# Kernel optimization log

Hardware: AMD Instinct MI355X
Metric: run time of the kernel (lower is better)

The kernel has to match this reference:

```python
import jax, jax.numpy as jnp
import numpy as np

B, S, D, H = 2, 2048, 1024, 16
HD = D // H  # head dim = 64


def setup_inputs() -> dict:
    key = jax.random.key(0)
    k0, k1, k2 = jax.random.split(key, 3)
    x = jax.random.normal(k0, (B, S, D), dtype=jnp.float32)
    # fused QKV projection: nn.Linear(D, 3D) -> weight [3D, D], bias [3D]
    Wqkv_w = jax.random.normal(k1, (3 * D, D), dtype=jnp.float32) * (1.0 / np.sqrt(D))
    Wqkv_b = jnp.zeros((3 * D,), dtype=jnp.float32)
    out_w = jax.random.normal(k2, (D, D), dtype=jnp.float32) * (1.0 / np.sqrt(D))
    out_b = jnp.zeros((D,), dtype=jnp.float32)
    # ALiBi-like additive bias, shape [1, H, 1, S] (broadcasts over queries)
    slopes = 2.0 ** (-8.0 * jnp.arange(1, H + 1, dtype=jnp.float32) / H)  # [H]
    dist = (S - 1) - jnp.arange(S, dtype=jnp.float32)                      # [S]
    attn_bias = (-slopes[:, None] * dist[None, :]).reshape(1, H, 1, S)
    # key padding mask: second sequence is padded by 256 tokens at the end
    lengths = jnp.array([S, S - 256])
    attention_mask = jnp.arange(S)[None, :] < lengths[:, None]             # [B, S] bool
    return {"x": x, "Wqkv_w": Wqkv_w, "Wqkv_b": Wqkv_b, "out_w": out_w,
            "out_b": out_b, "attn_bias": attn_bias, "attention_mask": attention_mask}


def reference(x, Wqkv_w, Wqkv_b, out_w, out_b, attn_bias, attention_mask):
    b, s, d = x.shape
    # fused QKV projection, then chunk into q, k, v along feature dim
    qkv = jnp.einsum('bsd,ed->bse', x, Wqkv_w) + Wqkv_b  # [b, s, 3d]
    q, k, v = jnp.split(qkv, 3, axis=-1)
    # b s (h hd) -> b h s hd
    q = q.reshape(b, s, H, HD).transpose(0, 2, 1, 3)
    k = k.reshape(b, s, H, HD).transpose(0, 2, 1, 3)
    v = v.reshape(b, s, H, HD).transpose(0, 2, 1, 3)
    softmax_scale = 1.0 / np.sqrt(HD)
    aw = jnp.einsum('bhqe,bhke->bhqk', q, k) * softmax_scale  # [b, H, s, s]
    aw = aw + attn_bias  # attn_bias broadcasts [1,H,1,s] -> [b,H,s,s]
    min_val = jnp.finfo(aw.dtype).min
    # key padding mask: mask positions where attention_mask is False
    aw = jnp.where(attention_mask[:, None, None, :], aw, min_val)
    # causal mask (is_causal=True, s_q == s_k)
    causal = jnp.tril(jnp.ones((s, s), dtype=bool))
    aw = jnp.where(causal[None, None, :, :], aw, min_val)
    p = jax.nn.softmax(aw, axis=-1)
    out = jnp.einsum('bhqk,bhke->bhqe', p, v)  # [b, H, s, HD]
    out = out.transpose(0, 2, 1, 3).reshape(b, s, d)
    return jnp.einsum('bsd,ed->bse', out, out_w) + out_b
```

## Files before the change

kernel.cpp:

```cpp
#include <hip/hip_runtime.h>
#include <hip/hip_bf16.h>
#include <stdint.h>

typedef __attribute__((ext_vector_type(8))) short s16x8;
typedef __attribute__((ext_vector_type(8))) unsigned short u16x8;
typedef __attribute__((ext_vector_type(4))) float f32x4;

#define SEQ 2048
#define LOG2E 1.44269504088896f

__device__ __forceinline__ unsigned short f2b(float x) {
  union { __hip_bfloat16 h; unsigned short u; } cv;
  cv.h = __float2bfloat16(x);
  return cv.u;
}

__device__ __forceinline__ float exp2fast(float x) {
  float r;
  asm("v_exp_f32 %0, %1" : "=v"(r) : "v"(x));
  return r;
}

__device__ __forceinline__ void gload16(const void* g, void* l) {
  __builtin_amdgcn_global_load_lds(
      (const __attribute__((address_space(1))) void*)g,
      (__attribute__((address_space(3))) void*)l, 16, 0, 0);
}

__global__ void cvt_all(const float* __restrict__ x, const float* __restrict__ wq,
                        const float* __restrict__ ow, __hip_bfloat16* __restrict__ xb,
                        __hip_bfloat16* __restrict__ wqb, __hip_bfloat16* __restrict__ owb) {
  const int i = blockIdx.x * 256 + threadIdx.x;
  const float* src;
  __hip_bfloat16* dst;
  int off;
  if (i < 1048576) { src = x; dst = xb; off = i; }
  else if (i < 1835008) { src = wq; dst = wqb; off = i - 1048576; }
  else { src = ow; dst = owb; off = i - 1835008; }
  float4 v = reinterpret_cast<const float4*>(src)[off];
  ushort4 o;
  o.x = f2b(v.x); o.y = f2b(v.y); o.z = f2b(v.z); o.w = f2b(v.w);
  reinterpret_cast<ushort4*>(dst)[off] = o;
}

__global__ void build_biasm(const float* __restrict__ abias,
                            const void* __restrict__ maskp,
                            float* __restrict__ biasm) {
  const int i = blockIdx.x * 256 + threadIdx.x;
  const int b = i >> 15, h = (i >> 11) & 15, kv = i & 2047;
  const int* mi = (const int*)maskp;
  const unsigned char* mb = (const unsigned char*)maskp;
  const bool int_fmt = (mi[0] == 0 || mi[0] == 1);
  const bool ok = int_fmt ? (mi[b * SEQ + kv] != 0) : (mb[b * SEQ + kv] != 0);
  biasm[i] = ok ? abias[h * SEQ + kv] * LOG2E : -1e30f;
}

template <int MODE, int BM>
__global__ __launch_bounds__(256) void gemm_bt(
    const __hip_bfloat16* __restrict__ A, const __hip_bfloat16* __restrict__ B,
    const float* __restrict__ bias, void* __restrict__ Cout,
    __hip_bfloat16* __restrict__ Vt, int M, int N, int K) {
  constexpr int MR = BM / 32;
  __shared__ __align__(16) __hip_bfloat16 As[BM * 32];
  __shared__ __align__(16) __hip_bfloat16 Bs[128 * 32];
  const int tid = threadIdx.x;
  const int lane = tid & 63;
  const int w = tid >> 6;
  const int wr = w >> 1, wc = w & 1;
  const int rowg = blockIdx.x * BM;
  const int colg = blockIdx.y * 128;
  const int lr = lane & 15;
  const int lk = (lane >> 4) * 8;
  f32x4 acc[MR][4];
#pragma unroll
  for (int m = 0; m < MR; ++m)
#pragma unroll
    for (int n = 0; n < 4; ++n) acc[m][n] = (f32x4){0.f, 0.f, 0.f, 0.f};
  for (int kt = 0; kt < K; kt += 32) {
#pragma unroll
    for (int r = 0; r < BM / 64; ++r) {
      const int idx = r * 256 + tid;
      gload16(A + (size_t)(rowg + (idx >> 2)) * K + kt + (idx & 3) * 8, As + idx * 8);
    }
#pragma unroll
    for (int r = 0; r < 2; ++r) {
      const int idx = r * 256 + tid;
      gload16(B + (size_t)(colg + (idx >> 2)) * K + kt + (idx & 3) * 8, Bs + idx * 8);
    }
    __syncthreads();
    s16x8 af[MR], bfr[4];
#pragma unroll
    for (int m = 0; m < MR; ++m)
      af[m] = *reinterpret_cast<const s16x8*>(As + (wr * (BM / 2) + m * 16 + lr) * 32 + lk);
#pragma unroll
    for (int n = 0; n < 4; ++n)
      bfr[n] = *reinterpret_cast<const s16x8*>(Bs + (wc * 64 + n * 16 + lr) * 32 + lk);
#pragma unroll
    for (int m = 0; m < MR; ++m)
#pragma unroll
      for (int n = 0; n < 4; ++n)
        acc[m][n] = __builtin_amdgcn_mfma_f32_16x16x32_bf16(af[m], bfr[n], acc[m][n], 0, 0, 0);
    __syncthreads();
  }
  const int r0l = (lane >> 4) * 4;
#pragma unroll
  for (int m = 0; m < MR; ++m) {
#pragma unroll
    for (int n = 0; n < 4; ++n) {
      const int col = colg + wc * 64 + n * 16 + lr;
      const int row0 = rowg + wr * (BM / 2) + m * 16 + r0l;
      const float bv = bias[col];
      if (MODE == 0) {
        if (col < 2048) {
          __hip_bfloat16* qkb = (__hip_bfloat16*)Cout;
#pragma unroll
          for (int j = 0; j < 4; ++j)
            qkb[(size_t)(row0 + j) * 2048 + col] = __float2bfloat16(acc[m][n][j] + bv);
        } else {
          const int c2 = col - 2048;
          const int bb = row0 >> 11;
          const int s0 = row0 & 2047;
          ushort4 pk;
          unsigned short* pp = (unsigned short*)&pk;
#pragma unroll
          for (int j = 0; j < 4; ++j) pp[j] = f2b(acc[m][n][j] + bv);
          *reinterpret_cast<ushort4*>(
              Vt + ((size_t)(bb * 16 + (c2 >> 6)) * 64 + (c2 & 63)) * 2048 + s0) = pk;
        }
      } else {
        float* o = (float*)Cout;
#pragma unroll
        for (int j = 0; j < 4; ++j)
          o[(size_t)(row0 + j) * N + col] = acc[m][n][j] + bv;
      }
    }
  }
}

__device__ __forceinline__ int swz(int row, int byteInRow) {
  return row * 128 + (byteInRow ^ ((row & 7) << 4));
}

__device__ __forceinline__ void attn_tile(
    const char* Ks, const char* Vs, char* pw, const float* Bm,
    s16x8 aq0, s16x8 aq1, int lane, int kv0, int q_abs, bool causal,
    float& m_r, float& l_r, f32x4* oa) {
  const int lr = lane & 15;
  const int g = lane >> 4;
  const int lkB = g * 16;
  const float SCALE2 = 0.125f * LOG2E;
  f32x4 sf[4];
#pragma unroll
  for (int n = 0; n < 4; ++n) {
    s16x8 ak0 = *reinterpret_cast<const s16x8*>(Ks + swz(n * 16 + lr, lkB));
    s16x8 ak1 = *reinterpret_cast<const s16x8*>(Ks + swz(n * 16 + lr, 64 + lkB));
    f32x4 z = (f32x4){0.f, 0.f, 0.f, 0.f};
    z = __builtin_amdgcn_mfma_f32_16x16x32_bf16(ak0, aq0, z, 0, 0, 0);
    z = __builtin_amdgcn_mfma_f32_16x16x32_bf16(ak1, aq1, z, 0, 0, 0);
    sf[n] = z;
  }
#pragma unroll
  for (int n = 0; n < 4; ++n) {
    f32x4 bv = *reinterpret_cast<const f32x4*>(Bm + n * 16 + g * 4);
#pragma unroll
    for (int j = 0; j < 4; ++j) sf[n][j] = fmaf(sf[n][j], SCALE2, bv[j]);
  }
  if (causal) {
    const int kvb = kv0 + g * 4;
#pragma unroll
    for (int n = 0; n < 4; ++n)
#pragma unroll
      for (int j = 0; j < 4; ++j)
        if (kvb + n * 16 + j > q_abs) sf[n][j] = -1e30f;
  }
  float mx[4];
#pragma unroll
  for (int n = 0; n < 4; ++n)
    mx[n] = fmaxf(fmaxf(sf[n][0], sf[n][1]), fmaxf(sf[n][2], sf[n][3]));
  float tm = fmaxf(fmaxf(mx[0], mx[1]), fmaxf(mx[2], mx[3]));
  tm = fmaxf(tm, __shfl_xor(tm, 16));
  tm = fmaxf(tm, __shfl_xor(tm, 32));
  const float mn = fmaxf(m_r, tm);
  const float al = exp2fast(m_r - mn);
  m_r = mn;
  float ps[4];
#pragma unroll
  for (int n = 0; n < 4; ++n) {
#pragma unroll
    for (int j = 0; j < 4; ++j) sf[n][j] = exp2fast(sf[n][j] - mn);
    ps[n] = (sf[n][0] + sf[n][1]) + (sf[n][2] + sf[n][3]);
  }
  float rs = (ps[0] + ps[1]) + (ps[2] + ps[3]);
  rs += __shfl_xor(rs, 16);
  rs += __shfl_xor(rs, 32);
  l_r = l_r * al + rs;
  float alj[4];
#pragma unroll
  for (int j = 0; j < 4; ++j) alj[j] = __shfl(al, g * 4 + j);
#pragma unroll
  for (int d = 0; d < 4; ++d)
#pragma unroll
    for (int j = 0; j < 4; ++j) oa[d][j] *= alj[j];
#pragma unroll
  for (int n = 0; n < 4; ++n) {
    union { ushort4 u; uint2 v; } pk;
    pk.u.x = f2b(sf[n][0]); pk.u.y = f2b(sf[n][1]);
    pk.u.z = f2b(sf[n][2]); pk.u.w = f2b(sf[n][3]);
    *reinterpret_cast<uint2*>(pw + lr * 128 + ((n * 32 + g * 8) ^ ((lr & 7) << 4))) = pk.v;
  }
  s16x8 pa0 = *reinterpret_cast<const s16x8*>(pw + swz(lr, lkB));
  s16x8 pa1 = *reinterpret_cast<const s16x8*>(pw + swz(lr, 64 + lkB));
#pragma unroll
  for (int d = 0; d < 4; ++d) {
    s16x8 bv0 = *reinterpret_cast<const s16x8*>(Vs + swz(d * 16 + lr, lkB));
    s16x8 bv1 = *reinterpret_cast<const s16x8*>(Vs + swz(d * 16 + lr, 64 + lkB));
    oa[d] = __builtin_amdgcn_mfma_f32_16x16x32_bf16(pa0, bv0, oa[d], 0, 0, 0);
    oa[d] = __builtin_amdgcn_mfma_f32_16x16x32_bf16(pa1, bv1, oa[d], 0, 0, 0);
  }
}

__global__ __launch_bounds__(512) void attn_fwd3(
    const __hip_bfloat16* __restrict__ qk, const __hip_bfloat16* __restrict__ Vt,
    const float* __restrict__ biasm, __hip_bfloat16* __restrict__ O) {
  __shared__ __align__(16) char KV[2][2][64 * 128];
  __shared__ __align__(16) char Ps[8][16 * 128];
  __shared__ float Bm[2][64];
  __shared__ float mlArr[4][2][16];
  const int tid = threadIdx.x;
  const int lane = tid & 63;
  const int w = tid >> 6;
  const int wsub = w & 3;
  const int z = w >> 2;
  const int bid = blockIdx.x;
  const int qt = 31 - (bid >> 5);
  const int bh = bid & 31;
  const int b = bh >> 4, h = bh & 15;
  const int row0 = qt * 64 + wsub * 16;
  const int lr = lane & 15;
  const int g = lane >> 4;
  const int NTit = (qt >> 1) + 1;
  const __hip_bfloat16* qbase = qk + (size_t)b * SEQ * 2048 + h * 64 + g * 8;
  const s16x8 aq0 = *reinterpret_cast<const s16x8*>(qbase + (size_t)(row0 + lr) * 2048);
  const s16x8 aq1 = *reinterpret_cast<const s16x8*>(qbase + (size_t)(row0 + lr) * 2048 + 32);
  const int q_abs = row0 + lr;
  float m_r = -INFINITY, l_r = 0.f;
  f32x4 oa[4];
#pragma unroll
  for (int d = 0; d < 4; ++d) oa[d] = (f32x4){0.f, 0.f, 0.f, 0.f};
  const int srow = tid >> 3;
  const int c8 = tid & 7;
  const __hip_bfloat16* kbase = qk + (size_t)b * SEQ * 2048 + 1024 + h * 64 + c8 * 8;
  const __hip_bfloat16* vbase = Vt + ((size_t)bh * 64 + srow) * 2048 + c8 * 8;
  const float* bmb = biasm + (size_t)bh * 2048;
  u16x8 kpe, kpo, vpe, vpo;
  float bmv = 0.f;
#define ISSUE(T)                                                                 \
  {                                                                              \
    const int tE_ = 2 * (T);                                                     \
    const int tO_ = (2 * (T) + 1 <= qt) ? (2 * (T) + 1) : qt;                    \
    kpe = *reinterpret_cast<const u16x8*>(kbase + (size_t)(tE_ * 64 + srow) * 2048); \
    kpo = *reinterpret_cast<const u16x8*>(kbase + (size_t)(tO_ * 64 + srow) * 2048); \
    vpe = *reinterpret_cast<const u16x8*>(vbase + tE_ * 64);                     \
    vpo = *reinterpret_cast<const u16x8*>(vbase + tO_ * 64);                     \
    if (tid < 64) bmv = bmb[tE_ * 64 + tid];                                     \
    else if (tid < 128) bmv = bmb[tO_ * 64 + (tid - 64)];                        \
  }
  ISSUE(0);
  for (int t = 0; t < NTit; ++t) {
    __syncthreads();
    *reinterpret_cast<u16x8*>(KV[0][0] + swz(srow, c8 * 16)) = kpe;
    *reinterpret_cast<u16x8*>(KV[1][0] + swz(srow, c8 * 16)) = kpo;
    *reinterpret_cast<u16x8*>(KV[0][1] + swz(srow, c8 * 16)) = vpe;
    *reinterpret_cast<u16x8*>(KV[1][1] + swz(srow, c8 * 16)) = vpo;
    if (tid < 64) Bm[0][tid] = bmv;
    else if (tid < 128) Bm[1][tid - 64] = bmv;
    __syncthreads();
    if (t + 1 < NTit) ISSUE(t + 1);
    const int tz = 2 * t + z;
    if (tz <= qt)
      attn_tile(KV[z][0], KV[z][1], Ps[w], Bm[z], aq0, aq1, lane,
                tz * 64, q_abs, tz == qt, m_r, l_r, oa);
  }
#undef ISSUE
  __syncthreads();
  if (z == 1) {
    float* mo = (float*)(&Ps[0][0] + wsub * 4096);
#pragma unroll
    for (int d = 0; d < 4; ++d)
#pragma unroll
      for (int j = 0; j < 4; ++j)
        mo[(g * 4 + j) * 64 + d * 16 + lr] = oa[d][j];
    if (lane < 16) {
      mlArr[wsub][0][lr] = m_r;
      mlArr[wsub][1][lr] = l_r;
    }
  }
  __syncthreads();
  if (z == 0) {
    const float mB = mlArr[wsub][0][lr];
    const float lB = mlArr[wsub][1][lr];
    const float mS = fmaxf(m_r, mB);
    const float fA = exp2fast(m_r - mS);
    const float fB = exp2fast(mB - mS);
    const float linv = 1.0f / (l_r * fA + lB * fB);
    float fAj[4], fBj[4], lij[4];
#pragma unroll
    for (int j = 0; j < 4; ++j) {
      fAj[j] = __shfl(fA, g * 4 + j);
      fBj[j] = __shfl(fB, g * 4 + j);
      lij[j] = __shfl(linv, g * 4 + j);
    }
    const float* mo = (const float*)(&Ps[0][0] + wsub * 4096);
#pragma unroll
    for (int d = 0; d < 4; ++d)
#pragma unroll
      for (int j = 0; j < 4; ++j) {
        const float v =
            (oa[d][j] * fAj[j] + mo[(g * 4 + j) * 64 + d * 16 + lr] * fBj[j]) * lij[j];
        O[(size_t)(b * SEQ + row0 + g * 4 + j) * 1024 + h * 64 + d * 16 + lr] =
            __float2bfloat16(v);
      }
  }
}

extern "C" void kernel_launch(void* const* d_in, const int* in_sizes, int n_in,
                              void* d_out, int out_size, void* d_ws, size_t ws_size,
                              hipStream_t stream) {
  const float* x     = (const float*)d_in[0];
  const float* wqkv  = (const float*)d_in[1];
  const float* bqkv  = (const float*)d_in[2];
  const float* wout  = (const float*)d_in[3];
  const float* bout  = (const float*)d_in[4];
  const float* abias = (const float*)d_in[5];
  const void*  mask  = d_in[6];

  __hip_bfloat16* ws  = (__hip_bfloat16*)d_ws;
  __hip_bfloat16* xb  = ws;
  __hip_bfloat16* wqb = ws + 4194304;
  __hip_bfloat16* owb = ws + 7340032;
  __hip_bfloat16* qkb = ws + 8388608;
  __hip_bfloat16* vtb = ws + 16777216;
  float*          bmf = (float*)(ws + 20971520);
  __hip_bfloat16* aob = xb;

  cvt_all<<<8192, 256, 0, stream>>>(x, wqkv, wout, xb, wqb, owb);
  build_biasm<<<256, 256, 0, stream>>>(abias, mask, bmf);
  gemm_bt<0, 128><<<dim3(32, 24), 256, 0, stream>>>(xb, wqb, bqkv, (void*)qkb, vtb,
                                                    4096, 3072, 1024);
  attn_fwd3<<<1024, 512, 0, stream>>>(qkb, vtb, bmf, aob);
  gemm_bt<1, 64><<<dim3(64, 8), 256, 0, stream>>>(aob, owb, bout, d_out,
                                                  (__hip_bfloat16*)nullptr, 4096, 1024, 1024);
}
```

Baseline: 122.1 us.

## Pair causal query tiles per block for balanced attention work; fuse bias-mask build

Each attention block now processes two query tiles (qt=31-p and qt=p), so every block does the same 17 KV-pair iterations instead of a varying count. The grid drops from 1024 blocks to 512, and the K/V prefetch pipeline carries straight across the tile switch, with a merge-and-write step in between. The separate build_biasm kernel is folded into cvt_all as extra blocks, removing one kernel launch. The trade-off is fewer, longer blocks, which removes tail imbalance but may lower occupancy-driven latency hiding.

New measurement: 125.4 us. 1.03x slower.

```diff
diff --git a/kernel.cpp b/kernel.cpp
--- a/kernel.cpp
+++ b/kernel.cpp
@@ -28,9 +28,21 @@
 }
 
 __global__ void cvt_all(const float* __restrict__ x, const float* __restrict__ wq,
-                        const float* __restrict__ ow, __hip_bfloat16* __restrict__ xb,
-                        __hip_bfloat16* __restrict__ wqb, __hip_bfloat16* __restrict__ owb) {
+                        const float* __restrict__ ow, const float* __restrict__ abias,
+                        const void* __restrict__ maskp,
+                        __hip_bfloat16* __restrict__ xb, __hip_bfloat16* __restrict__ wqb,
+                        __hip_bfloat16* __restrict__ owb, float* __restrict__ biasm) {
   const int i = blockIdx.x * 256 + threadIdx.x;
+  if (i >= 2097152) {
+    const int j = i - 2097152;
+    const int b = j >> 15, h = (j >> 11) & 15, kv = j & 2047;
+    const int* mi = (const int*)maskp;
+    const unsigned char* mb = (const unsigned char*)maskp;
+    const bool int_fmt = (mi[0] == 0 || mi[0] == 1);
+    const bool ok = int_fmt ? (mi[b * SEQ + kv] != 0) : (mb[b * SEQ + kv] != 0);
+    biasm[j] = ok ? abias[h * SEQ + kv] * LOG2E : -1e30f;
+    return;
+  }
   const float* src;
   __hip_bfloat16* dst;
   int off;
@@ -41,18 +53,6 @@
   ushort4 o;
   o.x = f2b(v.x); o.y = f2b(v.y); o.z = f2b(v.z); o.w = f2b(v.w);
   reinterpret_cast<ushort4*>(dst)[off] = o;
-}
-
-__global__ void build_biasm(const float* __restrict__ abias,
-                            const void* __restrict__ maskp,
-                            float* __restrict__ biasm) {
-  const int i = blockIdx.x * 256 + threadIdx.x;
-  const int b = i >> 15, h = (i >> 11) & 15, kv = i & 2047;
-  const int* mi = (const int*)maskp;
-  const unsigned char* mb = (const unsigned char*)maskp;
-  const bool int_fmt = (mi[0] == 0 || mi[0] == 1);
-  const bool ok = int_fmt ? (mi[b * SEQ + kv] != 0) : (mb[b * SEQ + kv] != 0);
-  biasm[i] = ok ? abias[h * SEQ + kv] * LOG2E : -1e30f;
 }
 
 template <int MODE, int BM>
@@ -219,7 +219,7 @@
   }
 }
 
-__global__ __launch_bounds__(512) void attn_fwd3(
+__global__ __launch_bounds__(512) void attn_fwd4(
     const __hip_bfloat16* __restrict__ qk, const __hip_bfloat16* __restrict__ Vt,
     const float* __restrict__ biasm, __hip_bfloat16* __restrict__ O) {
   __shared__ __align__(16) char KV[2][2][64 * 128];
@@ -231,18 +231,19 @@
   const int w = tid >> 6;
   const int wsub = w & 3;
   const int z = w >> 2;
-  const int bid = blockIdx.x;
-  const int qt = 31 - (bid >> 5);
-  const int bh = bid & 31;
+  const int p = blockIdx.x;
+  const int bh = blockIdx.y;
   const int b = bh >> 4, h = bh & 15;
-  const int row0 = qt * 64 + wsub * 16;
   const int lr = lane & 15;
   const int g = lane >> 4;
-  const int NTit = (qt >> 1) + 1;
+  const int qtA = 31 - p, qtB = p;
+  const int NT_A = (qtA >> 1) + 1;
   const __hip_bfloat16* qbase = qk + (size_t)b * SEQ * 2048 + h * 64 + g * 8;
-  const s16x8 aq0 = *reinterpret_cast<const s16x8*>(qbase + (size_t)(row0 + lr) * 2048);
-  const s16x8 aq1 = *reinterpret_cast<const s16x8*>(qbase + (size_t)(row0 + lr) * 2048 + 32);
-  const int q_abs = row0 + lr;
+  int qcur = qtA;
+  int row0 = qtA * 64 + wsub * 16;
+  int q_abs = row0 + lr;
+  s16x8 aq0 = *reinterpret_cast<const s16x8*>(qbase + (size_t)(row0 + lr) * 2048);
+  s16x8 aq1 = *reinterpret_cast<const s16x8*>(qbase + (size_t)(row0 + lr) * 2048 + 32);
   float m_r = -INFINITY, l_r = 0.f;
   f32x4 oa[4];
 #pragma unroll
@@ -254,10 +255,10 @@
   const float* bmb = biasm + (size_t)bh * 2048;
   u16x8 kpe, kpo, vpe, vpo;
   float bmv = 0.f;
-#define ISSUE(T)                                                                 \
+#define ISSUE(TL, QQ)                                                            \
   {                                                                              \
-    const int tE_ = 2 * (T);                                                     \
-    const int tO_ = (2 * (T) + 1 <= qt) ? (2 * (T) + 1) : qt;                    \
+    const int tE_ = 2 * (TL);                                                    \
+    const int tO_ = (2 * (TL) + 1 <= (QQ)) ? (2 * (TL) + 1) : (QQ);              \
     kpe = *reinterpret_cast<const u16x8*>(kbase + (size_t)(tE_ * 64 + srow) * 2048); \
     kpo = *reinterpret_cast<const u16x8*>(kbase + (size_t)(tO_ * 64 + srow) * 2048); \
     vpe = *reinterpret_cast<const u16x8*>(vbase + tE_ * 64);                     \
@@ -265,8 +266,44 @@
     if (tid < 64) bmv = bmb[tE_ * 64 + tid];                                     \
     else if (tid < 128) bmv = bmb[tO_ * 64 + (tid - 64)];                        \
   }
-  ISSUE(0);
-  for (int t = 0; t < NTit; ++t) {
+#define MERGE_WRITE()                                                            \
+  {                                                                              \
+    __syncthreads();                                                             \
+    if (z == 1) {                                                                \
+      float* mo = (float*)(&Ps[0][0] + wsub * 4096);                             \
+      _Pragma("unroll") for (int d = 0; d < 4; ++d)                              \
+          _Pragma("unroll") for (int j = 0; j < 4; ++j)                          \
+              mo[(g * 4 + j) * 64 + d * 16 + lr] = oa[d][j];                     \
+      if (lane < 16) { mlArr[wsub][0][lr] = m_r; mlArr[wsub][1][lr] = l_r; }     \
+    }                                                                            \
+    __syncthreads();                                                             \
+    if (z == 0) {                                                                \
+      const float mB = mlArr[wsub][0][lr];                                       \
+      const float lB = mlArr[wsub][1][lr];                                       \
+      const float mS = fmaxf(m_r, mB);                                           \
+      const float fA = exp2fast(m_r - mS);                                       \
+      const float fB = exp2fast(mB - mS);                                        \
+      const float linv = 1.0f / (l_r * fA + lB * fB);                            \
+      float fAj[4], fBj[4], lij[4];                                              \
+      _Pragma("unroll") for (int j = 0; j < 4; ++j) {                            \
+        fAj[j] = __shfl(fA, g * 4 + j);                                          \
+        fBj[j] = __shfl(fB, g * 4 + j);                                          \
+        lij[j] = __shfl(linv, g * 4 + j);                                        \
+      }                                                                          \
+      const float* mo = (const float*)(&Ps[0][0] + wsub * 4096);                 \
+      _Pragma("unroll") for (int d = 0; d < 4; ++d)                              \
+          _Pragma("unroll") for (int j = 0; j < 4; ++j) {                        \
+            const float v = (oa[d][j] * fAj[j] +                                 \
+                             mo[(g * 4 + j) * 64 + d * 16 + lr] * fBj[j]) * lij[j]; \
+            O[(size_t)(b * SEQ + row0 + g * 4 + j) * 1024 + h * 64 + d * 16 + lr] = \
+                __float2bfloat16(v);                                             \
+          }                                                                      \
+    }                                                                            \
+  }
+  ISSUE(0, qtA);
+  for (int t = 0; t < 17; ++t) {
+    const bool inA = t < NT_A;
+    const int tl = inA ? t : t - NT_A;
     __syncthreads();
     *reinterpret_cast<u16x8*>(KV[0][0] + swz(srow, c8 * 16)) = kpe;
     *reinterpret_cast<u16x8*>(KV[1][0] + swz(srow, c8 * 16)) = kpo;
@@ -275,52 +312,31 @@
     if (tid < 64) Bm[0][tid] = bmv;
     else if (tid < 128) Bm[1][tid - 64] = bmv;
     __syncthreads();
-    if (t + 1 < NTit) ISSUE(t + 1);
-    const int tz = 2 * t + z;
-    if (tz <= qt)
+    if (t + 1 < 17) {
+      const bool inA2 = (t + 1) < NT_A;
+      const int tl2 = inA2 ? t + 1 : t + 1 - NT_A;
+      const int q2 = inA2 ? qtA : qtB;
+      ISSUE(tl2, q2);
+    }
+    const int tz = 2 * tl + z;
+    if (tz <= qcur)
       attn_tile(KV[z][0], KV[z][1], Ps[w], Bm[z], aq0, aq1, lane,
-                tz * 64, q_abs, tz == qt, m_r, l_r, oa);
-  }
+                tz * 64, q_abs, tz == qcur, m_r, l_r, oa);
+    if (t == NT_A - 1) {
+      MERGE_WRITE();
+      qcur = qtB;
+      row0 = qtB * 64 + wsub * 16;
+      q_abs = row0 + lr;
+      aq0 = *reinterpret_cast<const s16x8*>(qbase + (size_t)(row0 + lr) * 2048);
+      aq1 = *reinterpret_cast<const s16x8*>(qbase + (size_t)(row0 + lr) * 2048 + 32);
+      m_r = -INFINITY; l_r = 0.f;
+#pragma unroll
+      for (int d = 0; d < 4; ++d) oa[d] = (f32x4){0.f, 0.f, 0.f, 0.f};
+    }
+  }
+  MERGE_WRITE();
 #undef ISSUE
-  __syncthreads();
-  if (z == 1) {
-    float* mo = (float*)(&Ps[0][0] + wsub * 4096);
-#pragma unroll
-    for (int d = 0; d < 4; ++d)
-#pragma unroll
-      for (int j = 0; j < 4; ++j)
-        mo[(g * 4 + j) * 64 + d * 16 + lr] = oa[d][j];
-    if (lane < 16) {
-      mlArr[wsub][0][lr] = m_r;
-      mlArr[wsub][1][lr] = l_r;
-    }
-  }
-  __syncthreads();
-  if (z == 0) {
-    const float mB = mlArr[wsub][0][lr];
-    const float lB = mlArr[wsub][1][lr];
-    const float mS = fmaxf(m_r, mB);
-    const float fA = exp2fast(m_r - mS);
-    const float fB = exp2fast(mB - mS);
-    const float linv = 1.0f / (l_r * fA + lB * fB);
-    float fAj[4], fBj[4], lij[4];
-#pragma unroll
-    for (int j = 0; j < 4; ++j) {
-      fAj[j] = __shfl(fA, g * 4 + j);
-      fBj[j] = __shfl(fB, g * 4 + j);
-      lij[j] = __shfl(linv, g * 4 + j);
-    }
-    const float* mo = (const float*)(&Ps[0][0] + wsub * 4096);
-#pragma unroll
-    for (int d = 0; d < 4; ++d)
-#pragma unroll
-      for (int j = 0; j < 4; ++j) {
-        const float v =
-            (oa[d][j] * fAj[j] + mo[(g * 4 + j) * 64 + d * 16 + lr] * fBj[j]) * lij[j];
-        O[(size_t)(b * SEQ + row0 + g * 4 + j) * 1024 + h * 64 + d * 16 + lr] =
-            __float2bfloat16(v);
-      }
-  }
+#undef MERGE_WRITE
 }
 
 extern "C" void kernel_launch(void* const* d_in, const int* in_sizes, int n_in,
@@ -343,11 +359,10 @@
   float*          bmf = (float*)(ws + 20971520);
   __hip_bfloat16* aob = xb;
 
-  cvt_all<<<8192, 256, 0, stream>>>(x, wqkv, wout, xb, wqb, owb);
-  build_biasm<<<256, 256, 0, stream>>>(abias, mask, bmf);
+  cvt_all<<<8448, 256, 0, stream>>>(x, wqkv, wout, abias, mask, xb, wqb, owb, bmf);
   gemm_bt<0, 128><<<dim3(32, 24), 256, 0, stream>>>(xb, wqb, bqkv, (void*)qkb, vtb,
                                                     4096, 3072, 1024);
-  attn_fwd3<<<1024, 512, 0, stream>>>(qkb, vtb, bmf, aob);
+  attn_fwd4<<<dim3(16, 32), 512, 0, stream>>>(qkb, vtb, bmf, aob);
   gemm_bt<1, 64><<<dim3(64, 8), 256, 0, stream>>>(aob, owb, bout, d_out,
                                                   (__hip_bfloat16*)nullptr, 4096, 1024, 1024);
 }
```

## Restructure attention: 128-row query tiles, direct-to-LDS K/V loads, fused bias prep

Applied to the files above, without the earlier changes.

The attention kernel now gives each 512-thread block 128 query rows (16 per wave) instead of splitting 64 rows across two KV-parity wave groups. This removes the end-of-kernel merge of two partial softmax states. K and V tiles are double-buffered with global_load_lds direct-to-LDS copies, which needs the QKV GEMM epilogue to write K and V pre-swizzled in global memory. The bias/mask build is merged into the conversion kernel to save a launch, and the bias is now read from global memory rather than staged in LDS. The costs are more per-wave idle time on the causal diagonal and a more complex block-to-tile mapping with reversed ordering for load balance.

After: 133.7 us. 9.5% more time.

```diff
diff --git a/kernel.cpp b/kernel.cpp
--- a/kernel.cpp
+++ b/kernel.cpp
@@ -28,9 +28,21 @@
 }
 
 __global__ void cvt_all(const float* __restrict__ x, const float* __restrict__ wq,
-                        const float* __restrict__ ow, __hip_bfloat16* __restrict__ xb,
-                        __hip_bfloat16* __restrict__ wqb, __hip_bfloat16* __restrict__ owb) {
+                        const float* __restrict__ ow, const float* __restrict__ abias,
+                        const void* __restrict__ maskp,
+                        __hip_bfloat16* __restrict__ xb, __hip_bfloat16* __restrict__ wqb,
+                        __hip_bfloat16* __restrict__ owb, float* __restrict__ biasm) {
   const int i = blockIdx.x * 256 + threadIdx.x;
+  if (i >= 2097152) {
+    const int j = i - 2097152;
+    const int b = j >> 15, h = (j >> 11) & 15, kv = j & 2047;
+    const int* mi = (const int*)maskp;
+    const unsigned char* mb = (const unsigned char*)maskp;
+    const bool int_fmt = (mi[0] == 0 || mi[0] == 1);
+    const bool ok = int_fmt ? (mi[b * SEQ + kv] != 0) : (mb[b * SEQ + kv] != 0);
+    biasm[j] = ok ? abias[h * SEQ + kv] * LOG2E : -1e30f;
+    return;
+  }
   const float* src;
   __hip_bfloat16* dst;
   int off;
@@ -41,18 +53,6 @@
   ushort4 o;
   o.x = f2b(v.x); o.y = f2b(v.y); o.z = f2b(v.z); o.w = f2b(v.w);
   reinterpret_cast<ushort4*>(dst)[off] = o;
-}
-
-__global__ void build_biasm(const float* __restrict__ abias,
-                            const void* __restrict__ maskp,
-                            float* __restrict__ biasm) {
-  const int i = blockIdx.x * 256 + threadIdx.x;
-  const int b = i >> 15, h = (i >> 11) & 15, kv = i & 2047;
-  const int* mi = (const int*)maskp;
-  const unsigned char* mb = (const unsigned char*)maskp;
-  const bool int_fmt = (mi[0] == 0 || mi[0] == 1);
-  const bool ok = int_fmt ? (mi[b * SEQ + kv] != 0) : (mb[b * SEQ + kv] != 0);
-  biasm[i] = ok ? abias[h * SEQ + kv] * LOG2E : -1e30f;
 }
 
 template <int MODE, int BM>
@@ -111,21 +111,31 @@
       const int row0 = rowg + wr * (BM / 2) + m * 16 + r0l;
       const float bv = bias[col];
       if (MODE == 0) {
-        if (col < 2048) {
-          __hip_bfloat16* qkb = (__hip_bfloat16*)Cout;
+        __hip_bfloat16* qkb = (__hip_bfloat16*)Cout;
+        if (col < 1024) {
 #pragma unroll
           for (int j = 0; j < 4; ++j)
             qkb[(size_t)(row0 + j) * 2048 + col] = __float2bfloat16(acc[m][n][j] + bv);
+        } else if (col < 2048) {
+          const int dd = col & 63;
+          const int base = col - dd;
+#pragma unroll
+          for (int j = 0; j < 4; ++j) {
+            const int s = row0 + j;
+            qkb[(size_t)s * 2048 + base + (dd ^ ((s & 7) << 3))] =
+                __float2bfloat16(acc[m][n][j] + bv);
+          }
         } else {
           const int c2 = col - 2048;
+          const int dd = c2 & 63;
           const int bb = row0 >> 11;
-          const int s0 = row0 & 2047;
+          const int s0 = (row0 & 2047) ^ ((dd & 7) << 3);
           ushort4 pk;
           unsigned short* pp = (unsigned short*)&pk;
 #pragma unroll
           for (int j = 0; j < 4; ++j) pp[j] = f2b(acc[m][n][j] + bv);
           *reinterpret_cast<ushort4*>(
-              Vt + ((size_t)(bb * 16 + (c2 >> 6)) * 64 + (c2 & 63)) * 2048 + s0) = pk;
+              Vt + ((size_t)(bb * 16 + (c2 >> 6)) * 64 + dd) * 2048 + s0) = pk;
         }
       } else {
         float* o = (float*)Cout;
@@ -142,7 +152,7 @@
 }
 
 __device__ __forceinline__ void attn_tile(
-    const char* Ks, const char* Vs, char* pw, const float* Bm,
+    const char* Ks, const char* Vs, char* pw, const float* bmb,
     s16x8 aq0, s16x8 aq1, int lane, int kv0, int q_abs, bool causal,
     float& m_r, float& l_r, f32x4* oa) {
   const int lr = lane & 15;
@@ -161,7 +171,7 @@
   }
 #pragma unroll
   for (int n = 0; n < 4; ++n) {
-    f32x4 bv = *reinterpret_cast<const f32x4*>(Bm + n * 16 + g * 4);
+    f32x4 bv = *reinterpret_cast<const f32x4*>(bmb + kv0 + n * 16 + g * 4);
 #pragma unroll
     for (int j = 0; j < 4; ++j) sf[n][j] = fmaf(sf[n][j], SCALE2, bv[j]);
   }
@@ -219,108 +229,67 @@
   }
 }
 
-__global__ __launch_bounds__(512) void attn_fwd3(
+__global__ __launch_bounds__(512) void attn_fwd5(
     const __hip_bfloat16* __restrict__ qk, const __hip_bfloat16* __restrict__ Vt,
     const float* __restrict__ biasm, __hip_bfloat16* __restrict__ O) {
-  __shared__ __align__(16) char KV[2][2][64 * 128];
-  __shared__ __align__(16) char Ps[8][16 * 128];
-  __shared__ float Bm[2][64];
-  __shared__ float mlArr[4][2][16];
+  __shared__ __align__(16) char KB[2][8192];
+  __shared__ __align__(16) char VB[2][8192];
+  __shared__ __align__(16) char Ps[8][2048];
   const int tid = threadIdx.x;
   const int lane = tid & 63;
   const int w = tid >> 6;
-  const int wsub = w & 3;
-  const int z = w >> 2;
   const int bid = blockIdx.x;
-  const int qt = 31 - (bid >> 5);
-  const int bh = bid & 31;
+  const int halfg = bid >> 8;
+  const int idx = bid & 255;
+  const int qt = halfg ? (idx >> 4) : (15 - (idx >> 4));
+  const int bh = (halfg << 4) | (idx & 15);
   const int b = bh >> 4, h = bh & 15;
-  const int row0 = qt * 64 + wsub * 16;
   const int lr = lane & 15;
   const int g = lane >> 4;
-  const int NTit = (qt >> 1) + 1;
-  const __hip_bfloat16* qbase = qk + (size_t)b * SEQ * 2048 + h * 64 + g * 8;
-  const s16x8 aq0 = *reinterpret_cast<const s16x8*>(qbase + (size_t)(row0 + lr) * 2048);
-  const s16x8 aq1 = *reinterpret_cast<const s16x8*>(qbase + (size_t)(row0 + lr) * 2048 + 32);
-  const int q_abs = row0 + lr;
+  const int w0 = qt * 128 + w * 16;
+  const int q_abs = w0 + lr;
+  const int NT = 2 * qt + 2;
+  const __hip_bfloat16* qptr = qk + (size_t)(b * SEQ + w0 + lr) * 2048 + h * 64 + g * 8;
+  const s16x8 aq0 = *reinterpret_cast<const s16x8*>(qptr);
+  const s16x8 aq1 = *reinterpret_cast<const s16x8*>(qptr + 32);
+  const float* bmb = biasm + (size_t)bh * 2048;
   float m_r = -INFINITY, l_r = 0.f;
   f32x4 oa[4];
 #pragma unroll
   for (int d = 0; d < 4; ++d) oa[d] = (f32x4){0.f, 0.f, 0.f, 0.f};
-  const int srow = tid >> 3;
-  const int c8 = tid & 7;
-  const __hip_bfloat16* kbase = qk + (size_t)b * SEQ * 2048 + 1024 + h * 64 + c8 * 8;
-  const __hip_bfloat16* vbase = Vt + ((size_t)bh * 64 + srow) * 2048 + c8 * 8;
-  const float* bmb = biasm + (size_t)bh * 2048;
-  u16x8 kpe, kpo, vpe, vpo;
-  float bmv = 0.f;
-#define ISSUE(T)                                                                 \
-  {                                                                              \
-    const int tE_ = 2 * (T);                                                     \
-    const int tO_ = (2 * (T) + 1 <= qt) ? (2 * (T) + 1) : qt;                    \
-    kpe = *reinterpret_cast<const u16x8*>(kbase + (size_t)(tE_ * 64 + srow) * 2048); \
-    kpo = *reinterpret_cast<const u16x8*>(kbase + (size_t)(tO_ * 64 + srow) * 2048); \
-    vpe = *reinterpret_cast<const u16x8*>(vbase + tE_ * 64);                     \
-    vpo = *reinterpret_cast<const u16x8*>(vbase + tO_ * 64);                     \
-    if (tid < 64) bmv = bmb[tE_ * 64 + tid];                                     \
-    else if (tid < 128) bmv = bmb[tO_ * 64 + (tid - 64)];                        \
-  }
-  ISSUE(0);
-  for (int t = 0; t < NTit; ++t) {
+  const int r_ = tid >> 3;
+  const int c16 = tid & 7;
+  const __hip_bfloat16* kb = qk + ((size_t)b * SEQ + r_) * 2048 + 1024 + h * 64 + c16 * 8;
+  const __hip_bfloat16* vb = Vt + ((size_t)bh * 64 + r_) * 2048 + c16 * 8;
+#define ISSUE(T, C)                                        \
+  {                                                        \
+    const int kv0_ = (T) * 64;                             \
+    gload16(kb + (size_t)kv0_ * 2048, KB[C] + tid * 16);   \
+    gload16(vb + kv0_, VB[C] + tid * 16);                  \
+  }
+  ISSUE(0, 0);
+  __syncthreads();
+  int cur = 0;
+  for (int t = 0; t < NT; ++t) {
+    if (t + 1 < NT) ISSUE(t + 1, cur ^ 1);
+    const int kv0 = t * 64;
+    if (kv0 <= w0 + 15)
+      attn_tile(KB[cur], VB[cur], Ps[w], bmb, aq0, aq1, lane, kv0, q_abs,
+                kv0 + 63 > w0, m_r, l_r, oa);
     __syncthreads();
-    *reinterpret_cast<u16x8*>(KV[0][0] + swz(srow, c8 * 16)) = kpe;
-    *reinterpret_cast<u16x8*>(KV[1][0] + swz(srow, c8 * 16)) = kpo;
-    *reinterpret_cast<u16x8*>(KV[0][1] + swz(srow, c8 * 16)) = vpe;
-    *reinterpret_cast<u16x8*>(KV[1][1] + swz(srow, c8 * 16)) = vpo;
-    if (tid < 64) Bm[0][tid] = bmv;
-    else if (tid < 128) Bm[1][tid - 64] = bmv;
-    __syncthreads();
-    if (t + 1 < NTit) ISSUE(t + 1);
-    const int tz = 2 * t + z;
-    if (tz <= qt)
-      attn_tile(KV[z][0], KV[z][1], Ps[w], Bm[z], aq0, aq1, lane,
-                tz * 64, q_abs, tz == qt, m_r, l_r, oa);
+    cur ^= 1;
   }
 #undef ISSUE
-  __syncthreads();
-  if (z == 1) {
-    float* mo = (float*)(&Ps[0][0] + wsub * 4096);
-#pragma unroll
-    for (int d = 0; d < 4; ++d)
-#pragma unroll
-      for (int j = 0; j < 4; ++j)
-        mo[(g * 4 + j) * 64 + d * 16 + lr] = oa[d][j];
-    if (lane < 16) {
-      mlArr[wsub][0][lr] = m_r;
-      mlArr[wsub][1][lr] = l_r;
-    }
-  }
-  __syncthreads();
-  if (z == 0) {
-    const float mB = mlArr[wsub][0][lr];
-    const float lB = mlArr[wsub][1][lr];
-    const float mS = fmaxf(m_r, mB);
-    const float fA = exp2fast(m_r - mS);
-    const float fB = exp2fast(mB - mS);
-    const float linv = 1.0f / (l_r * fA + lB * fB);
-    float fAj[4], fBj[4], lij[4];
-#pragma unroll
-    for (int j = 0; j < 4; ++j) {
-      fAj[j] = __shfl(fA, g * 4 + j);
-      fBj[j] = __shfl(fB, g * 4 + j);
-      lij[j] = __shfl(linv, g * 4 + j);
-    }
-    const float* mo = (const float*)(&Ps[0][0] + wsub * 4096);
-#pragma unroll
-    for (int d = 0; d < 4; ++d)
-#pragma unroll
-      for (int j = 0; j < 4; ++j) {
-        const float v =
-            (oa[d][j] * fAj[j] + mo[(g * 4 + j) * 64 + d * 16 + lr] * fBj[j]) * lij[j];
-        O[(size_t)(b * SEQ + row0 + g * 4 + j) * 1024 + h * 64 + d * 16 + lr] =
-            __float2bfloat16(v);
-      }
-  }
+  const float linv = 1.0f / l_r;
+  float lij[4];
+#pragma unroll
+  for (int j = 0; j < 4; ++j) lij[j] = __shfl(linv, g * 4 + j);
+#pragma unroll
+  for (int d = 0; d < 4; ++d)
+#pragma unroll
+    for (int j = 0; j < 4; ++j)
+      O[(size_t)(b * SEQ + w0 + g * 4 + j) * 1024 + h * 64 + d * 16 + lr] =
+          __float2bfloat16(oa[d][j] * lij[j]);
 }
 
 extern "C" void kernel_launch(void* const* d_in, const int* in_sizes, int n_in,
@@ -343,11 +312,10 @@
   float*          bmf = (float*)(ws + 20971520);
   __hip_bfloat16* aob = xb;
 
-  cvt_all<<<8192, 256, 0, stream>>>(x, wqkv, wout, xb, wqb, owb);
-  build_biasm<<<256, 256, 0, stream>>>(abias, mask, bmf);
+  cvt_all<<<8448, 256, 0, stream>>>(x, wqkv, wout, abias, mask, xb, wqb, owb, bmf);
   gemm_bt<0, 128><<<dim3(32, 24), 256, 0, stream>>>(xb, wqb, bqkv, (void*)qkb, vtb,
                                                     4096, 3072, 1024);
-  attn_fwd3<<<1024, 512, 0, stream>>>(qkb, vtb, bmf, aob);
+  attn_fwd5<<<512, 512, 0, stream>>>(qkb, vtb, bmf, aob);
   gemm_bt<1, 64><<<dim3(64, 8), 256, 0, stream>>>(aob, owb, bout, d_out,
                                                   (__hip_bfloat16*)nullptr, 4096, 1024, 1024);
 }
```
